# Performance work log

Hardware: AMD Instinct MI355X
Metric: run time of the kernel (lower is better)

The kernel has to match this reference:

```python
import jax, jax.numpy as jnp
import numpy as np

NUM_CLASSES = 80
INPUT_SHAPE = (416.0, 416.0)
ANCHORS_MASK0 = np.array([6, 7, 8])
CONF_THRES = 0.5
NMS_THRES = 0.4
IMAGE_SHAPE = (416.0, 416.0)
MAX_DET = 100          # fixed-size padded NMS output (jit-compatible)
CLASS_OFFSET = 4096.0  # class-aware box offset == independent per-class NMS
NEG = jnp.float32(-1e9)


def setup_inputs() -> dict:
    key = jax.random.key(0)
    inputs_1 = jax.random.normal(key, (32, 255, 52, 52), dtype=jnp.float32)
    anchors = jnp.array([[10, 13], [16, 30], [33, 23], [30, 61], [62, 45],
                         [59, 119], [116, 90], [156, 198], [373, 326]], dtype=jnp.float32)
    return {"inputs_1": inputs_1, "anchors": anchors}


def _decode(inputs_1, anchors):
    B, C, H, W = inputs_1.shape
    A = len(ANCHORS_MASK0)
    attrs = C // A  # 5 + num_classes
    # [B, A, H, W, attrs]
    pred = inputs_1.reshape(B, A, attrs, H, W).transpose(0, 1, 3, 4, 2)
    xy = jax.nn.sigmoid(pred[..., 0:2])
    wh = pred[..., 2:4]
    conf = jax.nn.sigmoid(pred[..., 4])
    cls = jax.nn.sigmoid(pred[..., 5:])
    stride_h = INPUT_SHAPE[0] / H
    stride_w = INPUT_SHAPE[1] / W
    anc = anchors[ANCHORS_MASK0] / jnp.array([stride_w, stride_h], jnp.float32)  # [A,2]
    gx = jnp.arange(W, dtype=jnp.float32)
    gy = jnp.arange(H, dtype=jnp.float32)
    bx = xy[..., 0] + gx[None, None, None, :]
    by = xy[..., 1] + gy[None, None, :, None]
    bw = jnp.exp(wh[..., 0]) * anc[:, 0][None, :, None, None]
    bh = jnp.exp(wh[..., 1]) * anc[:, 1][None, :, None, None]
    boxes = jnp.stack([bx, by, bw, bh], -1) / jnp.array([W, H, W, H], jnp.float32)
    return jnp.concatenate([boxes.reshape(B, -1, 4),
                            conf.reshape(B, -1, 1),
                            cls.reshape(B, -1, NUM_CLASSES)], axis=-1)  # [B, A*H*W, 5+C]


def _iou(box, boxes):
    lt = jnp.maximum(box[:2], boxes[:, :2])
    rb = jnp.minimum(box[2:], boxes[:, 2:])
    wh = jnp.clip(rb - lt, 0.0)
    inter = wh[:, 0] * wh[:, 1]
    a1 = (box[2] - box[0]) * (box[3] - box[1])
    a2 = (boxes[:, 2] - boxes[:, 0]) * (boxes[:, 3] - boxes[:, 1])
    return inter / (a1 + a2 - inter + 1e-9)


def _nms(pred0):
    # pred0: [N, 5+C] (image 0, matching torch code which only processes prediction[0])
    cx, cy, w, h = pred0[:, 0], pred0[:, 1], pred0[:, 2], pred0[:, 3]
    corners = jnp.stack([cx - w / 2, cy - h / 2, cx + w / 2, cy + h / 2], -1)  # [N,4]
    class_conf = jnp.max(pred0[:, 5:], axis=1)
    class_pred = jnp.argmax(pred0[:, 5:], axis=1)
    score = pred0[:, 4] * class_conf  # obj_conf * class_conf, same score nms() receives
    valid = score >= CONF_THRES
    # offsetting boxes by class id makes a single NMS pass equivalent to the per-class loop
    obox = corners + (class_pred.astype(jnp.float32) * CLASS_OFFSET)[:, None]
    s0 = jnp.where(valid, score, NEG)

    def step(scores, _):
        i = jnp.argmax(scores)
        flag = scores[i] > NEG / 2
        iou = _iou(obox[i], obox)
        new_scores = jnp.where(iou > NMS_THRES, NEG, scores).at[i].set(NEG)
        return new_scores, (i, flag)

    _, (idxs, flags) = jax.lax.scan(step, s0, None, length=MAX_DET)
    det = jnp.concatenate([
        corners[idxs],                                  # x1,y1,x2,y2
        pred0[idxs, 4:5],                               # obj conf
        class_conf[idxs][:, None],                      # class conf
        class_pred[idxs].astype(jnp.float32)[:, None],  # class id
    ], axis=1)  # [MAX_DET, 7]
    # yolo_correct_boxes: xywh -> yx min/max scaled to image_shape
    box_xy = (det[:, 0:2] + det[:, 2:4]) / 2.0
    box_wh = det[:, 2:4] - det[:, 0:2]
    box_yx = box_xy[:, ::-1]
    box_hw = box_wh[:, ::-1]
    mins = box_yx - box_hw / 2.0
    maxes = box_yx + box_hw / 2.0
    scale = jnp.array([IMAGE_SHAPE[0], IMAGE_SHAPE[1], IMAGE_SHAPE[0], IMAGE_SHAPE[1]], jnp.float32)
    boxes_corr = jnp.concatenate([mins, maxes], axis=1) * scale
    det = jnp.concatenate([boxes_corr, det[:, 4:]], axis=1)
    return det * flags[:, None].astype(jnp.float32)  # zero-padded rows where no detection


def reference(inputs_1, anchors):
    out = _decode(inputs_1, anchors)   # [B, 3*H*W, 5+num_classes]
    det = _nms(out[0])                 # [MAX_DET, 7], padded fixed-size NMS result
    return (out, det)
```

## Files before the change

### kernel.cpp

```cpp
#include <hip/hip_runtime.h>
#include <math.h>

constexpr int An = 3;
constexpr int Wd = 52;
constexpr int HWn = 2704;
constexpr int ATT = 85;
constexpr int CH = 208;
constexpr int PITCH = 212;
constexpr int CHUNKS = 13;
constexpr int DEC_BLOCKS = 96 * CHUNKS;
constexpr int NC = An * HWn;
constexpr int OUT_DEC = 32 * NC * ATT;
constexpr float NEGV = -1.0e9f;
constexpr int WS_SCORE_OFF = 65536;
constexpr size_t DEC_LDS = (size_t)ATT * PITCH * sizeof(float);

__device__ __forceinline__ float sig_(float x) {
    return 1.0f / (1.0f + expf(-x));
}

__global__ void __launch_bounds__(128)
yolo_prep(const float* __restrict__ in, const float* __restrict__ anc,
          float* __restrict__ ws)
{
    const int n = blockIdx.x * 128 + threadIdx.x;
    if (n >= NC) return;
    const int a   = n / HWn;
    const int pos = n - a * HWn;
    const float* p = in + (size_t)a * 85 * HWn + pos;

    const float tx = p[0];
    const float ty = p[HWn];
    const float tw = p[2 * HWn];
    const float th = p[3 * HWn];
    const float tc = p[4 * HWn];

    float m = -3.0e38f; int cp = 0;
    #pragma unroll
    for (int j0 = 0; j0 < 80; j0 += 16) {
        float v[16];
        #pragma unroll
        for (int u = 0; u < 16; ++u) v[u] = p[(size_t)(5 + j0 + u) * HWn];
        #pragma unroll
        for (int u = 0; u < 16; ++u) {
            if (v[u] > m) { m = v[u]; cp = j0 + u; }
        }
    }

    const float cc    = sig_(m);
    const float conf  = sig_(tc);
    const float score = __fmul_rn(conf, cc);
    const float aw = anc[(6 + a) * 2 + 0] * 0.125f;
    const float ah = anc[(6 + a) * 2 + 1] * 0.125f;
    const float cx = (sig_(tx) + (float)(pos % Wd)) / 52.0f;
    const float cy = (sig_(ty) + (float)(pos / Wd)) / 52.0f;
    const float bw = expf(tw) * aw / 52.0f;
    const float bh = expf(th) * ah / 52.0f;
    const float hw = __fmul_rn(bw, 0.5f);
    const float hh = __fmul_rn(bh, 0.5f);
    float4* w4 = (float4*)ws;
    w4[2 * n + 0] = make_float4(__fsub_rn(cx, hw), __fsub_rn(cy, hh),
                                __fadd_rn(cx, hw), __fadd_rn(cy, hh));
    w4[2 * n + 1] = make_float4(conf, cc, (float)cp, 0.0f);
    ws[WS_SCORE_OFF + n] = score;
}

__global__ void __launch_bounds__(1024)
yolo_fused(const float* __restrict__ in, const float* __restrict__ anc,
           float* __restrict__ out, const float* __restrict__ ws)
{
    extern __shared__ float dynsm[];
    const int tid = threadIdx.x;

    if (blockIdx.x != 0) {
        const int bi    = (int)blockIdx.x - 1;
        const int chunk = bi % CHUNKS;
        const int ba    = bi / CHUNKS;
        const int a     = ba % An;
        const float anc_w = anc[(6 + a) * 2 + 0] * 0.125f;
        const float anc_h = anc[(6 + a) * 2 + 1] * 0.125f;
        const int pos0  = chunk * CH;
        const float* src = in + (size_t)ba * 85 * HWn + pos0;
        const float gy0 = (float)(chunk * 4);

        for (int i = tid; i < ATT * 52; i += 1024) {
            const int attr = i / 52;
            const int q    = i - attr * 52;
            const float4 x = *(const float4*)(src + (size_t)attr * HWn + 4 * q);
            const float xs[4] = {x.x, x.y, x.z, x.w};
            float v[4];
            #pragma unroll
            for (int u = 0; u < 4; ++u) {
                const int pp = 4 * q + u;
                float val;
                if (attr >= 4)      val = sig_(xs[u]);
                else if (attr == 0) val = (sig_(xs[u]) + (float)(pp % 52)) / 52.0f;
                else if (attr == 1) val = (sig_(xs[u]) + (gy0 + (float)(pp / 52))) / 52.0f;
                else if (attr == 2) val = expf(xs[u]) * anc_w / 52.0f;
                else                val = expf(xs[u]) * anc_h / 52.0f;
                v[u] = val;
            }
            *(float4*)(dynsm + attr * PITCH + 4 * q) = make_float4(v[0], v[1], v[2], v[3]);
        }
        __syncthreads();

        float* dst = out + ((size_t)ba * HWn + pos0) * ATT;
        for (int j = tid; j < ATT * 52; j += 1024) {
            const int f0 = 4 * j;
            float v[4];
            #pragma unroll
            for (int u = 0; u < 4; ++u) {
                const int g  = f0 + u;
                const int p  = g / 85;
                const int at = g - 85 * p;
                v[u] = dynsm[at * PITCH + p];
            }
            *(float4*)(dst + f0) = make_float4(v[0], v[1], v[2], v[3]);
        }
        return;
    }

    unsigned long long* keys = (unsigned long long*)dynsm;
    float* kept     = dynsm + 16384;
    float* detstage = kept + 400;
    float* winslot  = detstage + 700;
    int*   wavemin  = (int*)(winslot + 8);
    int*   meta     = wavemin + 16;
    const int lane = tid & 63;
    const int wv   = tid >> 6;

    if (tid == 0) meta[0] = 0;
    __syncthreads();

    const float* wscore = ws + WS_SCORE_OFF;
    for (int k = 0; k < 8; ++k) {
        const int n = tid + k * 1024;
        const float s = (n < NC) ? wscore[n] : NEGV;
        const bool valid = (s >= 0.5f);
        const unsigned long long mask = __ballot(valid);
        if (mask != 0ULL) {
            const int leader = __ffsll((long long)mask) - 1;
            int base = 0;
            if (lane == leader) base = atomicAdd(&meta[0], __popcll(mask));
            base = __shfl(base, leader);
            if (valid) {
                const int slot = base + __popcll(mask & ((1ULL << lane) - 1ULL));
                keys[slot] =
                    ((unsigned long long)(0xFFFFFFFFu - __float_as_uint(s)) << 32)
                    | (unsigned)n;
            }
        }
    }
    __syncthreads();
    const int V = meta[0];
    int P2 = 1; while (P2 < V) P2 <<= 1;
    for (int i = V + tid; i < P2; i += 1024) keys[i] = ~0ULL;
    __syncthreads();

    for (int k = 2; k <= P2; k <<= 1) {
        for (int j = k >> 1; j > 0; j >>= 1) {
            for (int idx = tid; idx < (P2 >> 1); idx += 1024) {
                const int i = ((idx & ~(j - 1)) << 1) | (idx & (j - 1));
                const int l = i | j;
                const unsigned long long a = keys[i], b = keys[l];
                const bool up = ((i & k) == 0);
                if (up ? (b < a) : (a < b)) { keys[i] = b; keys[l] = a; }
            }
            __syncthreads();
        }
    }

    const float4* w4 = (const float4*)ws;
    float4* keptv = (float4*)kept;
    int nk = 0;
    for (int sb = 0; sb * 1024 < V && nk < 100; ++sb) {
        const int cidx = sb * 1024 + tid;
        const bool act = (cidx < V);
        float rx1 = 0, ry1 = 0, rx2 = 0, ry2 = 0, mconf = 0, mcc = 0, mcp = 0;
        float ox1 = 0, oy1 = 0, ox2 = 0, oy2 = 0, aC = 0;
        bool alive = act;
        if (act) {
            const int n = (int)(keys[cidx] & 0xFFFFFFFFu);
            const float4 bx = w4[2 * n], mt = w4[2 * n + 1];
            rx1 = bx.x; ry1 = bx.y; rx2 = bx.z; ry2 = bx.w;
            mconf = mt.x; mcc = mt.y; mcp = mt.z;
            const float off = __fmul_rn(mcp, 4096.0f);
            ox1 = __fadd_rn(rx1, off); oy1 = __fadd_rn(ry1, off);
            ox2 = __fadd_rn(rx2, off); oy2 = __fadd_rn(ry2, off);
            aC  = __fmul_rn(__fsub_rn(ox2, ox1), __fsub_rn(oy2, oy1));
            for (int t = 0; t < nk && alive; ++t) {
                const float4 kb = keptv[t];
                const float ltx = fmaxf(kb.x, ox1), lty = fmaxf(kb.y, oy1);
                const float rbx = fminf(kb.z, ox2), rby = fminf(kb.w, oy2);
                const float iw = fmaxf(__fsub_rn(rbx, ltx), 0.0f);
                const float ih = fmaxf(__fsub_rn(rby, lty), 0.0f);
                const float inter = __fmul_rn(iw, ih);
                const float aK = __fmul_rn(__fsub_rn(kb.z, kb.x), __fsub_rn(kb.w, kb.y));
                const float den = __fadd_rn(__fsub_rn(__fadd_rn(aK, aC), inter), 1e-9f);
                if (inter / den > 0.4f) alive = false;
            }
        }
        if (tid == 0) {
            winslot[0] = 4e9f; winslot[1] = 4e9f; winslot[2] = 4e9f; winslot[3] = 4e9f;
            winslot[4] = 0.0f;
        }
        __syncthreads();

        while (true) {
            if (alive) {
                const float wx1 = winslot[0], wy1 = winslot[1];
                const float wx2 = winslot[2], wy2 = winslot[3], aW = winslot[4];
                const float ltx = fmaxf(wx1, ox1), lty = fmaxf(wy1, oy1);
                const float rbx = fminf(wx2, ox2), rby = fminf(wy2, oy2);
                const float iw = fmaxf(__fsub_rn(rbx, ltx), 0.0f);
                const float ih = fmaxf(__fsub_rn(rby, lty), 0.0f);
                const float inter = __fmul_rn(iw, ih);
                const float den = __fadd_rn(__fsub_rn(__fadd_rn(aW, aC), inter), 1e-9f);
                if (inter / den > 0.4f) alive = false;
            }
            const unsigned long long m = __ballot(alive);
            if (lane == 0)
                wavemin[wv] = m ? (wv * 64 + (__ffsll((long long)m) - 1)) : 0x7FFFFFFF;
            __syncthreads();
            int win = 0x7FFFFFFF;
            #pragma unroll
            for (int w = 0; w < 16; ++w) win = min(win, wavemin[w]);
            if (win == 0x7FFFFFFF) break;
            if (tid == win) {
                winslot[0] = ox1; winslot[1] = oy1; winslot[2] = ox2; winslot[3] = oy2;
                winslot[4] = aC;
                keptv[nk] = make_float4(ox1, oy1, ox2, oy2);
                float* dr = detstage + nk * 7;
                const float xm  = __fmul_rn(__fadd_rn(rx1, rx2), 0.5f);
                const float ym  = __fmul_rn(__fadd_rn(ry1, ry2), 0.5f);
                const float hw2 = __fmul_rn(__fsub_rn(rx2, rx1), 0.5f);
                const float hh2 = __fmul_rn(__fsub_rn(ry2, ry1), 0.5f);
                dr[0] = __fmul_rn(__fsub_rn(ym, hh2), 416.0f);
                dr[1] = __fmul_rn(__fsub_rn(xm, hw2), 416.0f);
                dr[2] = __fmul_rn(__fadd_rn(ym, hh2), 416.0f);
                dr[3] = __fmul_rn(__fadd_rn(xm, hw2), 416.0f);
                dr[4] = mconf; dr[5] = mcc; dr[6] = mcp;
                alive = false;
            }
            __syncthreads();
            ++nk;
            if (nk == 100) break;
        }
    }
    __syncthreads();

    for (int i = tid; i < 100 * 7; i += 1024) {
        out[OUT_DEC + i] = (i < nk * 7) ? detstage[i] : 0.0f;
    }
}

extern "C" void kernel_launch(void* const* d_in, const int* in_sizes, int n_in,
                              void* d_out, int out_size, void* d_ws, size_t ws_size,
                              hipStream_t stream) {
    const float* in  = (const float*)d_in[0];
    const float* anc = (const float*)d_in[1];
    float* out = (float*)d_out;
    float* ws  = (float*)d_ws;

    hipLaunchKernelGGL(yolo_prep, dim3((NC + 127) / 128), dim3(128), 0, stream,
                       in, anc, ws);
    hipLaunchKernelGGL(yolo_fused, dim3(DEC_BLOCKS + 1), dim3(1024), DEC_LDS,
                       stream, in, anc, out, ws);
}
```

Before: 235.6 us.

## Split NMS and decode kernels, halve NMS barriers, use fast exp in decode

Splits the former fused kernel into a single-block NMS kernel and a separate decode kernel, launched one after the other on the same stream. The NMS kernel stores each candidate box in LDS and double-buffers the per-wave minima, so the greedy suppression loop needs one barrier per kept box instead of two. The decode kernel switches to scalar loads and stores, an odd LDS pitch meant to avoid bank conflicts, and __expf for the sigmoid and exp terms. In exchange, decode can no longer overlap with NMS, it gives up vectorised memory access, and its results lose some precision.

```diff
diff --git a/kernel.cpp b/kernel.cpp
--- a/kernel.cpp
+++ b/kernel.cpp
@@ -6,17 +6,32 @@
 constexpr int HWn = 2704;
 constexpr int ATT = 85;
 constexpr int CH = 208;
-constexpr int PITCH = 212;
+constexpr int PITCH = 209;
 constexpr int CHUNKS = 13;
 constexpr int DEC_BLOCKS = 96 * CHUNKS;
 constexpr int NC = An * HWn;
 constexpr int OUT_DEC = 32 * NC * ATT;
 constexpr float NEGV = -1.0e9f;
 constexpr int WS_SCORE_OFF = 65536;
+constexpr int INFI = 0x7FFFFFFF;
 constexpr size_t DEC_LDS = (size_t)ATT * PITCH * sizeof(float);
 
-__device__ __forceinline__ float sig_(float x) {
+constexpr int L_BX1  = 16384;
+constexpr int L_BY1  = 17408;
+constexpr int L_BX2  = 18432;
+constexpr int L_BY2  = 19456;
+constexpr int L_BAR  = 20480;
+constexpr int L_KEPT = 21504;
+constexpr int L_DET  = 21904;
+constexpr int L_WMIN = 22604;
+constexpr int L_META = 22636;
+constexpr size_t NMS_LDS = 22640u * sizeof(float);
+
+__device__ __forceinline__ float sig_precise(float x) {
     return 1.0f / (1.0f + expf(-x));
+}
+__device__ __forceinline__ float sig_fast(float x) {
+    return 1.0f / (1.0f + __expf(-x));
 }
 
 __global__ void __launch_bounds__(128)
@@ -47,13 +62,13 @@
         }
     }
 
-    const float cc    = sig_(m);
-    const float conf  = sig_(tc);
+    const float cc    = sig_precise(m);
+    const float conf  = sig_precise(tc);
     const float score = __fmul_rn(conf, cc);
     const float aw = anc[(6 + a) * 2 + 0] * 0.125f;
     const float ah = anc[(6 + a) * 2 + 1] * 0.125f;
-    const float cx = (sig_(tx) + (float)(pos % Wd)) / 52.0f;
-    const float cy = (sig_(ty) + (float)(pos / Wd)) / 52.0f;
+    const float cx = (sig_precise(tx) + (float)(pos % Wd)) / 52.0f;
+    const float cy = (sig_precise(ty) + (float)(pos / Wd)) / 52.0f;
     const float bw = expf(tw) * aw / 52.0f;
     const float bh = expf(th) * ah / 52.0f;
     const float hw = __fmul_rn(bw, 0.5f);
@@ -66,66 +81,18 @@
 }
 
 __global__ void __launch_bounds__(1024)
-yolo_fused(const float* __restrict__ in, const float* __restrict__ anc,
-           float* __restrict__ out, const float* __restrict__ ws)
+yolo_nms(const float* __restrict__ ws, float* __restrict__ out)
 {
-    extern __shared__ float dynsm[];
-    const int tid = threadIdx.x;
-
-    if (blockIdx.x != 0) {
-        const int bi    = (int)blockIdx.x - 1;
-        const int chunk = bi % CHUNKS;
-        const int ba    = bi / CHUNKS;
-        const int a     = ba % An;
-        const float anc_w = anc[(6 + a) * 2 + 0] * 0.125f;
-        const float anc_h = anc[(6 + a) * 2 + 1] * 0.125f;
-        const int pos0  = chunk * CH;
-        const float* src = in + (size_t)ba * 85 * HWn + pos0;
-        const float gy0 = (float)(chunk * 4);
-
-        for (int i = tid; i < ATT * 52; i += 1024) {
-            const int attr = i / 52;
-            const int q    = i - attr * 52;
-            const float4 x = *(const float4*)(src + (size_t)attr * HWn + 4 * q);
-            const float xs[4] = {x.x, x.y, x.z, x.w};
-            float v[4];
-            #pragma unroll
-            for (int u = 0; u < 4; ++u) {
-                const int pp = 4 * q + u;
-                float val;
-                if (attr >= 4)      val = sig_(xs[u]);
-                else if (attr == 0) val = (sig_(xs[u]) + (float)(pp % 52)) / 52.0f;
-                else if (attr == 1) val = (sig_(xs[u]) + (gy0 + (float)(pp / 52))) / 52.0f;
-                else if (attr == 2) val = expf(xs[u]) * anc_w / 52.0f;
-                else                val = expf(xs[u]) * anc_h / 52.0f;
-                v[u] = val;
-            }
-            *(float4*)(dynsm + attr * PITCH + 4 * q) = make_float4(v[0], v[1], v[2], v[3]);
-        }
-        __syncthreads();
-
-        float* dst = out + ((size_t)ba * HWn + pos0) * ATT;
-        for (int j = tid; j < ATT * 52; j += 1024) {
-            const int f0 = 4 * j;
-            float v[4];
-            #pragma unroll
-            for (int u = 0; u < 4; ++u) {
-                const int g  = f0 + u;
-                const int p  = g / 85;
-                const int at = g - 85 * p;
-                v[u] = dynsm[at * PITCH + p];
-            }
-            *(float4*)(dst + f0) = make_float4(v[0], v[1], v[2], v[3]);
-        }
-        return;
-    }
-
-    unsigned long long* keys = (unsigned long long*)dynsm;
-    float* kept     = dynsm + 16384;
-    float* detstage = kept + 400;
-    float* winslot  = detstage + 700;
-    int*   wavemin  = (int*)(winslot + 8);
-    int*   meta     = wavemin + 16;
+    extern __shared__ float sm[];
+    unsigned long long* keys = (unsigned long long*)sm;
+    float* lx1 = sm + L_BX1;  float* ly1 = sm + L_BY1;
+    float* lx2 = sm + L_BX2;  float* ly2 = sm + L_BY2;
+    float* lar = sm + L_BAR;
+    float4* keptv   = (float4*)(sm + L_KEPT);
+    float* detstage = sm + L_DET;
+    int*   wavemin  = (int*)(sm + L_WMIN);
+    int*   meta     = (int*)(sm + L_META);
+    const int tid  = threadIdx.x;
     const int lane = tid & 63;
     const int wv   = tid >> 6;
 
@@ -171,15 +138,13 @@
     }
 
     const float4* w4 = (const float4*)ws;
-    float4* keptv = (float4*)kept;
     int nk = 0;
-    for (int sb = 0; sb * 1024 < V && nk < 100; ++sb) {
-        const int cidx = sb * 1024 + tid;
-        const bool act = (cidx < V);
+    for (int base = 0; base < V && nk < 100; base += 1024) {
+        const int cidx = base + tid;
+        bool alive = (cidx < V);
         float rx1 = 0, ry1 = 0, rx2 = 0, ry2 = 0, mconf = 0, mcc = 0, mcp = 0;
         float ox1 = 0, oy1 = 0, ox2 = 0, oy2 = 0, aC = 0;
-        bool alive = act;
-        if (act) {
+        if (alive) {
             const int n = (int)(keys[cidx] & 0xFFFFFFFFu);
             const float4 bx = w4[2 * n], mt = w4[2 * n + 1];
             rx1 = bx.x; ry1 = bx.y; rx2 = bx.z; ry2 = bx.w;
@@ -188,6 +153,8 @@
             ox1 = __fadd_rn(rx1, off); oy1 = __fadd_rn(ry1, off);
             ox2 = __fadd_rn(rx2, off); oy2 = __fadd_rn(ry2, off);
             aC  = __fmul_rn(__fsub_rn(ox2, ox1), __fsub_rn(oy2, oy1));
+            lx1[tid] = ox1; ly1[tid] = oy1; lx2[tid] = ox2; ly2[tid] = oy2;
+            lar[tid] = aC;
             for (int t = 0; t < nk && alive; ++t) {
                 const float4 kb = keptv[t];
                 const float ltx = fmaxf(kb.x, ox1), lty = fmaxf(kb.y, oy1);
@@ -200,35 +167,20 @@
                 if (inter / den > 0.4f) alive = false;
             }
         }
-        if (tid == 0) {
-            winslot[0] = 4e9f; winslot[1] = 4e9f; winslot[2] = 4e9f; winslot[3] = 4e9f;
-            winslot[4] = 0.0f;
-        }
-        __syncthreads();
-
+
+        int it = 0;
         while (true) {
-            if (alive) {
-                const float wx1 = winslot[0], wy1 = winslot[1];
-                const float wx2 = winslot[2], wy2 = winslot[3], aW = winslot[4];
-                const float ltx = fmaxf(wx1, ox1), lty = fmaxf(wy1, oy1);
-                const float rbx = fminf(wx2, ox2), rby = fminf(wy2, oy2);
-                const float iw = fmaxf(__fsub_rn(rbx, ltx), 0.0f);
-                const float ih = fmaxf(__fsub_rn(rby, lty), 0.0f);
-                const float inter = __fmul_rn(iw, ih);
-                const float den = __fadd_rn(__fsub_rn(__fadd_rn(aW, aC), inter), 1e-9f);
-                if (inter / den > 0.4f) alive = false;
-            }
-            const unsigned long long m = __ballot(alive);
+            const unsigned long long mb = __ballot(alive);
             if (lane == 0)
-                wavemin[wv] = m ? (wv * 64 + (__ffsll((long long)m) - 1)) : 0x7FFFFFFF;
+                wavemin[(it & 1) * 16 + wv] =
+                    mb ? (wv * 64 + (__ffsll((long long)mb) - 1)) : INFI;
             __syncthreads();
-            int win = 0x7FFFFFFF;
+            int win = INFI;
             #pragma unroll
-            for (int w = 0; w < 16; ++w) win = min(win, wavemin[w]);
-            if (win == 0x7FFFFFFF) break;
+            for (int w = 0; w < 16; ++w)
+                win = min(win, wavemin[(it & 1) * 16 + w]);
+            if (win == INFI) break;
             if (tid == win) {
-                winslot[0] = ox1; winslot[1] = oy1; winslot[2] = ox2; winslot[3] = oy2;
-                winslot[4] = aC;
                 keptv[nk] = make_float4(ox1, oy1, ox2, oy2);
                 float* dr = detstage + nk * 7;
                 const float xm  = __fmul_rn(__fadd_rn(rx1, rx2), 0.5f);
@@ -242,15 +194,64 @@
                 dr[4] = mconf; dr[5] = mcc; dr[6] = mcp;
                 alive = false;
             }
-            __syncthreads();
             ++nk;
             if (nk == 100) break;
-        }
-    }
-    __syncthreads();
+            if (alive) {
+                const float wx1 = lx1[win], wy1 = ly1[win];
+                const float wx2 = lx2[win], wy2 = ly2[win], aW = lar[win];
+                const float ltx = fmaxf(wx1, ox1), lty = fmaxf(wy1, oy1);
+                const float rbx = fminf(wx2, ox2), rby = fminf(wy2, oy2);
+                const float iw = fmaxf(__fsub_rn(rbx, ltx), 0.0f);
+                const float ih = fmaxf(__fsub_rn(rby, lty), 0.0f);
+                const float inter = __fmul_rn(iw, ih);
+                const float den = __fadd_rn(__fsub_rn(__fadd_rn(aW, aC), inter), 1e-9f);
+                if (inter / den > 0.4f) alive = false;
+            }
+            ++it;
+        }
+        __syncthreads();
+    }
 
     for (int i = tid; i < 100 * 7; i += 1024) {
         out[OUT_DEC + i] = (i < nk * 7) ? detstage[i] : 0.0f;
+    }
+}
+
+__global__ void __launch_bounds__(1024)
+yolo_decode(const float* __restrict__ in, const float* __restrict__ anc,
+            float* __restrict__ out)
+{
+    extern __shared__ float smem[];
+    const int tid = threadIdx.x;
+    const int bi    = (int)blockIdx.x;
+    const int chunk = bi % CHUNKS;
+    const int ba    = bi / CHUNKS;
+    const int a     = ba % An;
+    const float anc_w = anc[(6 + a) * 2 + 0] * 0.125f;
+    const float anc_h = anc[(6 + a) * 2 + 1] * 0.125f;
+    const int pos0  = chunk * CH;
+    const float* src = in + (size_t)ba * 85 * HWn + pos0;
+
+    for (int i = tid; i < ATT * CH; i += 1024) {
+        const int attr = i / CH;
+        const int p    = i - attr * CH;
+        const int pos  = pos0 + p;
+        const float x  = src[(size_t)attr * HWn + p];
+        float v;
+        if (attr >= 4)      v = sig_fast(x);
+        else if (attr == 0) v = (sig_fast(x) + (float)(pos % Wd)) / 52.0f;
+        else if (attr == 1) v = (sig_fast(x) + (float)(pos / Wd)) / 52.0f;
+        else if (attr == 2) v = __expf(x) * anc_w / 52.0f;
+        else                v = __expf(x) * anc_h / 52.0f;
+        smem[attr * PITCH + p] = v;
+    }
+    __syncthreads();
+
+    float* dst = out + ((size_t)ba * HWn + pos0) * ATT;
+    for (int f = tid; f < CH * ATT; f += 1024) {
+        const int p    = f / ATT;
+        const int attr = f - p * ATT;
+        dst[f] = smem[attr * PITCH + p];
     }
 }
 
@@ -264,6 +265,7 @@
 
     hipLaunchKernelGGL(yolo_prep, dim3((NC + 127) / 128), dim3(128), 0, stream,
                        in, anc, ws);
-    hipLaunchKernelGGL(yolo_fused, dim3(DEC_BLOCKS + 1), dim3(1024), DEC_LDS,
-                       stream, in, anc, out, ws);
-}
+    hipLaunchKernelGGL(yolo_nms, dim3(1), dim3(1024), NMS_LDS, stream, ws, out);
+    hipLaunchKernelGGL(yolo_decode, dim3(DEC_BLOCKS), dim3(1024), DEC_LDS, stream,
+                       in, anc, out);
+}
```

New measurement: 290.3 us. 1.23x slower.
